# Performance work log

Measured on AMD Instinct MI355X. Metric: run time of the kernel, lower is better.

## Reference

```python
import jax, jax.numpy as jnp
import numpy as np

B, LC, LE, H, V = 128, 256, 257, 512, 128
PAD = 0  # padding_token_index


def lstm_cell(x, h, c, Wih, Whh, b):
    # torch LSTMCell gate order: i, f, g, o
    g = x @ Wih.T + h @ Whh.T + b
    i, f, gg, o = jnp.split(g, 4, axis=-1)
    c = jax.nn.sigmoid(f) * c + jax.nn.sigmoid(i) * jnp.tanh(gg)
    h = jax.nn.sigmoid(o) * jnp.tanh(c)
    return h, c


def setup_inputs() -> dict:
    key = jax.random.key(0)
    ks = jax.random.split(key, 32)
    p = lambda k, shape: jax.random.normal(k, shape, jnp.float32) * 0.05
    d = {
        'C_idx': jax.random.randint(ks[0], (B, LC), 0, V, dtype=jnp.int32),
        'E_idx': jax.random.randint(ks[1], (B, LE), 0, V, dtype=jnp.int32),
        'C_pad': jnp.zeros((B, LC), dtype=bool),
        'enc_Wih_f': p(ks[2], (4 * H, V)),
        'enc_Whh_f': p(ks[3], (4 * H, H)),
        'enc_b_f': p(ks[4], (4 * H,)),
        'enc_Wih_b': p(ks[5], (4 * H, V)),
        'enc_Whh_b': p(ks[6], (4 * H, H)),
        'enc_b_b': p(ks[7], (4 * H,)),
        'dec_Wih': p(ks[8], (4 * H, H + V)),
        'dec_Whh': p(ks[9], (4 * H, H)),
        'dec_b': p(ks[10], (4 * H,)),
        'Wh': p(ks[11], (H, 2 * H)),
        'Wc': p(ks[12], (H, 2 * H)),
        'Wattn': p(ks[13], (H, 2 * H)),
        'Wout': p(ks[14], (H, 3 * H)),
        'Wvocab': p(ks[15], (V, H)),
        'pg_ctx': p(ks[16], (2 * H,)),
        'pg_in': p(ks[17], (V + H,)),
        'pg_h': p(ks[18], (H,)),
        'pg_c': p(ks[19], (H,)),
        'pg_b': p(ks[20], (1,)),
    }
    return d


def _forward(C_idx, E_idx, C_pad, enc_Wih_f, enc_Whh_f, enc_b_f, enc_Wih_b, enc_Whh_b, enc_b_b,
             dec_Wih, dec_Whh, dec_b, Wh, Wc, Wattn, Wout, Wvocab,
             pg_ctx, pg_in, pg_h, pg_c, pg_b):
    C = jax.nn.one_hot(C_idx, V, dtype=jnp.float32)      # [B,LC,V]
    E_emb = jax.nn.one_hot(E_idx, V, dtype=jnp.float32)  # [B,LE,V]
    z = jnp.zeros((B, H), jnp.float32)

    xs = jnp.swapaxes(C, 0, 1)  # [LC,B,V]

    def enc_fwd(carry, x):
        h, c = lstm_cell(x, carry[0], carry[1], enc_Wih_f, enc_Whh_f, enc_b_f)
        return (h, c), h

    def enc_bwd(carry, x):
        h, c = lstm_cell(x, carry[0], carry[1], enc_Wih_b, enc_Whh_b, enc_b_b)
        return (h, c), h

    (hf, cf), Hf = jax.lax.scan(enc_fwd, (z, z), xs)
    (hb, cb), Hb = jax.lax.scan(enc_bwd, (z, z), xs[::-1])
    Hb = Hb[::-1]
    enc = jnp.swapaxes(jnp.concatenate([Hf, Hb], axis=-1), 0, 1)  # [B,LC,2H]

    # decoder init state from final encoder states (fwd;bwd concat)
    h0 = jnp.concatenate([hf, hb], axis=-1) @ Wh.T
    c0 = jnp.concatenate([cf, cb], axis=-1) @ Wc.T

    enc_proj = enc @ Wattn.T  # [B,LC,H]

    def step(carry, x_emb):
        h, c, prev_out = carry
        nin = jnp.concatenate([x_emb, prev_out], axis=1)  # [B,V+H]
        h, c = lstm_cell(nin, h, c, dec_Wih, dec_Whh, dec_b)
        scores = jnp.einsum('blh,bh->bl', enc_proj, h)
        scores = jnp.where(C_pad, -jnp.inf, scores)
        attn = jax.nn.softmax(scores, axis=1)             # [B,LC]
        ctx = jnp.einsum('bl,blh->bh', attn, enc)         # [B,2H]
        t_out = jnp.tanh(jnp.concatenate([h, ctx], axis=1) @ Wout.T)  # [B,H]
        gen = jax.nn.softmax(t_out @ Wvocab.T, axis=1)    # [B,V]
        p_gen = jax.nn.sigmoid(ctx @ pg_ctx + nin @ pg_in + h @ pg_h + c @ pg_c + pg_b[0])[:, None]
        copy_p = attn * (1.0 - p_gen)
        out = jax.vmap(lambda o, idx, a: o.at[idx].add(a))(gen * p_gen, C_idx, copy_p)
        return (h, c, t_out), out

    xs2 = jnp.swapaxes(E_emb[:, :LE - 1], 0, 1)  # teacher inputs, step 0 = start token
    _, preds = jax.lax.scan(step, (h0, c0, z), xs2)
    preds = jnp.swapaxes(preds, 0, 1)  # [B,LE-1,V]

    tgt = E_idx[:, 1:]
    nll = -jnp.take_along_axis(jnp.log(preds), tgt[..., None], axis=2)[..., 0]
    return jnp.where(tgt == PAD, 0.0, nll)  # [B,LE-1], reduction='none'


def reference(C_idx, E_idx, C_pad, enc_Wih_f, enc_Whh_f, enc_b_f, enc_Wih_b, enc_Whh_b, enc_b_b,
              dec_Wih, dec_Whh, dec_b, Wh, Wc, Wattn, Wout, Wvocab,
              pg_ctx, pg_in, pg_h, pg_c, pg_b):
    return _forward(C_idx, E_idx, C_pad, enc_Wih_f, enc_Whh_f, enc_b_f, enc_Wih_b, enc_Whh_b, enc_b_b,
                    dec_Wih, dec_Whh, dec_b, Wh, Wc, Wattn, Wout, Wvocab,
                    pg_ctx, pg_in, pg_h, pg_c, pg_b)
```

## Files before the change

kernel.cpp:

```cpp
#include <hip/hip_runtime.h>

static constexpr size_t OFF_ENC   = 0;
static constexpr size_t OFF_WGE   = 67108864;
static constexpr size_t OFF_WIHTE = 71303168;
static constexpr size_t OFF_HENC  = 72351744;
static constexpr size_t OFF_CENC  = 72876032;
static constexpr size_t OFF_WGATE = 67108864;
static constexpr size_t OFF_XDEC  = 71303168;
static constexpr size_t OFF_WATTT = 71827456;
static constexpr size_t OFF_WOUT  = 72876032;
static constexpr size_t OFF_WVOCT = 74448896;
static constexpr size_t OFF_HDEC  = 74579968;
static constexpr size_t OFF_CDEC  = 74842112;
static constexpr size_t OFF_TOUT  = 75104256;
static constexpr size_t OFF_UFB   = 75366400;
static constexpr size_t OFF_CTXF  = 75628544;
static constexpr size_t OFF_CTXP  = 75890688;
static constexpr size_t OFF_SC    = 76414976;
static constexpr size_t OFF_MSP   = 76480512;
static constexpr size_t OFF_MD    = 76482560;

__device__ __forceinline__ float sigm(float x) { return 1.f / (1.f + expf(-x)); }
__device__ __forceinline__ unsigned short f2bf(float f) {
  unsigned u = __float_as_uint(f);
  u += 0x7fffu + ((u >> 16) & 1u);
  return (unsigned short)(u >> 16);
}
__device__ __forceinline__ float bfl(unsigned w) { return __uint_as_float(w << 16); }
__device__ __forceinline__ float bfh(unsigned w) { return __uint_as_float(w & 0xffff0000u); }
__device__ __forceinline__ float bf2f(unsigned short v) { return __uint_as_float(((unsigned)v) << 16); }

#if defined(__has_builtin)
// ... 6 lines not shown
__device__ __forceinline__ float dot2bf(unsigned w, unsigned h, float acc) {
  return __builtin_amdgcn_fdot2_f32_bf16(__builtin_bit_cast(bf2_t, w),
                                         __builtin_bit_cast(bf2_t, h), acc, false);
}
#else
__device__ __forceinline__ float dot2bf(unsigned w, unsigned h, float acc) {
  return acc + bfl(w) * bfl(h) + bfh(w) * bfh(h);
}
#endif

__global__ __launch_bounds__(256) void k_pre1(const float* __restrict__ WhhF,
                                              const float* __restrict__ WhhB,
                                              const float* __restrict__ WihF,
                                              const float* __restrict__ WihB,
                                              char* __restrict__ wsb) {
  unsigned short* WGE = (unsigned short*)(wsb + OFF_WGE);
  unsigned short* WIH = (unsigned short*)(wsb + OFF_WIHTE);
  int id = blockIdx.x * 256 + threadIdx.x, str = gridDim.x * 256;
  for (int x = id; x < 2 * 2048 * 512; x += str) {
    int dir = x >> 20, r = (x >> 9) & 2047, k = x & 511;
    const float* W = dir ? WhhB : WhhF;
    WGE[x] = f2bf(W[(size_t)r * 512 + k]);
  }
  for (int x = id; x < 2 * 128 * 2048; x += str) {
    int dir = x >> 18, v = (x >> 11) & 127, r = x & 2047;
    const float* W = dir ? WihB : WihF;
    WIH[x] = f2bf(W[(size_t)r * 128 + v]);
  }
}

__global__ __launch_bounds__(256) void k_pre2(const float* __restrict__ dWih,
                                              const float* __restrict__ dWhh,
                                              const float* __restrict__ Wattn,
                                              const float* __restrict__ Wout,
                                              const float* __restrict__ Wvoc,
                                              char* __restrict__ wsb) {
  unsigned short* WG = (unsigned short*)(wsb + OFF_WGATE);
  unsigned short* XD = (unsigned short*)(wsb + OFF_XDEC);
  unsigned short* WA = (unsigned short*)(wsb + OFF_WATTT);
  unsigned short* WO = (unsigned short*)(wsb + OFF_WOUT);
  unsigned*       WV = (unsigned*)(wsb + OFF_WVOCT);
  int id = blockIdx.x * 256 + threadIdx.x, str = gridDim.x * 256;
  for (int x = id; x < 2048 * 1024; x += str) {
// ... 6 lines not shown
    XD[x] = f2bf(dWih[(size_t)r * 640 + v]);
  }
  for (int x = id; x < 1024 * 512; x += str) {
    int i = x >> 9, o = x & 511;
    WA[x] = f2bf(Wattn[(size_t)o * 1024 + i]);
  }
  for (int x = id; x < 512 * 1536; x += str) WO[x] = f2bf(Wout[x]);
  for (int x = id; x < 256 * 128; x += str) {
    int kk = x >> 7, v = x & 127;
    unsigned lo = f2bf(Wvoc[(size_t)v * 512 + 2 * kk]);
    unsigned hi = f2bf(Wvoc[(size_t)v * 512 + 2 * kk + 1]);
    WV[x] = lo | (hi << 16);
  }
}

__global__ __launch_bounds__(512) void k_encs(const float* __restrict__ bF,
                                              const float* __restrict__ bB,
                                              const int* __restrict__ C_idx,
                                              char* __restrict__ wsb, int t) {
  int tau = threadIdx.x, bid = blockIdx.x;
  int b = tau & 127, slot = tau >> 7;
  int dir = bid >> 7;
  int j = __builtin_amdgcn_readfirstlane(((bid & 127) << 2) + slot);
  int dd = __builtin_amdgcn_readfirstlane(dir);
  int rp = t & 1, wp = rp ^ 1;
  const unsigned* inw = (const unsigned*)(wsb + OFF_HENC) + ((size_t)(dd * 2 + rp) * 256) * 128 + b;
  const uint4* w0 = (const uint4*)((const unsigned*)(wsb + OFF_WGE) + ((size_t)dd * 2048 + j) * 256);
  const uint4* w1 = (const uint4*)((const unsigned*)(wsb + OFF_WGE) + ((size_t)dd * 2048 + 512 + j) * 256);
  const uint4* w2 = (const uint4*)((const unsigned*)(wsb + OFF_WGE) + ((size_t)dd * 2048 + 1024 + j) * 256);
  const uint4* w3 = (const uint4*)((const unsigned*)(wsb + OFF_WGE) + ((size_t)dd * 2048 + 1536 + j) * 256);
  int l = dd ? (255 - t) : t;
  int cidx = C_idx[b * 256 + l];
  const unsigned short* xg = (const unsigned short*)(wsb + OFF_WIHTE) + ((size_t)dd * 128 + cidx) * 2048;
  const float* bias = dd ? bB : bF;
  float a0 = bias[j] + bf2f(xg[j]);
  float a1 = bias[512 + j] + bf2f(xg[512 + j]);
  float a2 = bias[1024 + j] + bf2f(xg[1024 + j]);
  float a3 = bias[1536 + j] + bf2f(xg[1536 + j]);
#pragma unroll 4
  for (int q = 0; q < 64; ++q) {
    uint4 W0 = w0[q], W1 = w1[q], W2 = w2[q], W3 = w3[q];
    unsigned i0 = inw[(q * 4 + 0) * 128], i1 = inw[(q * 4 + 1) * 128];
    unsigned i2 = inw[(q * 4 + 2) * 128], i3 = inw[(q * 4 + 3) * 128];
    a0 = dot2bf(W0.x, i0, a0); a0 = dot2bf(W0.y, i1, a0); a0 = dot2bf(W0.z, i2, a0); a0 = dot2bf(W0.w, i3, a0);
    a1 = dot2bf(W1.x, i0, a1); a1 = dot2bf(W1.y, i1, a1); a1 = dot2bf(W1.z, i2, a1); a1 = dot2bf(W1.w, i3, a1);
    a2 = dot2bf(W2.x, i0, a2); a2 = dot2bf(W2.y, i1, a2); a2 = dot2bf(W2.z, i2, a2); a2 = dot2bf(W2.w, i3, a2);
    a3 = dot2bf(W3.x, i0, a3); a3 = dot2bf(W3.y, i1, a3); a3 = dot2bf(W3.z, i2, a3); a3 = dot2bf(W3.w, i3, a3);
  }
  float ig = sigm(a0), fg = sigm(a1), gg = tanhf(a2), og = sigm(a3);
  float* cp = (float*)(wsb + OFF_CENC) + ((size_t)dir * 512 + j) * 128 + b;
  float c = fg * (*cp) + ig * gg;
  *cp = c;
  float h = og * tanhf(c);
  unsigned short hb = f2bf(h);
  ((unsigned short*)(wsb + OFF_HENC))[((((size_t)(dir * 2 + wp) * 256) + (j >> 1)) * 128 + b) * 2 + (j & 1)] = hb;
  ((unsigned short*)(wsb + OFF_ENC))[((size_t)b * 256 + l) * 1024 + dir * 512 + j] = hb;
}

__global__ __launch_bounds__(512) void k_h0(const float* __restrict__ Wh,
                                            const float* __restrict__ Wc,
                                            char* __restrict__ wsb) {
  int tau = threadIdx.x;
  int b = tau & 127, slot = tau >> 7;
  int row = __builtin_amdgcn_readfirstlane(blockIdx.x * 4 + slot);
  int sel = row >> 9, j = row & 511;
  const float* W = (sel ? Wc : Wh) + (size_t)j * 1024;
  const unsigned short* HE = (const unsigned short*)(wsb + OFF_HENC);
  const float* CE = (const float*)(wsb + OFF_CENC);
  float acc = 0.f;
  for (int k = 0; k < 1024; ++k) {
    int dir = k >> 9, k5 = k & 511;
    float in;
    if (sel == 0)
      in = bf2f(HE[((((size_t)(dir * 2 + 0) * 256) + (k5 >> 1)) * 128 + b) * 2 + (k5 & 1)]);
    else
      in = CE[((size_t)dir * 512 + k5) * 128 + b];
    acc += W[k] * in;
  }
  if (sel == 0)
    ((unsigned short*)(wsb + OFF_HDEC))[(((size_t)(j >> 1)) * 128 + b) * 2 + (j & 1)] = f2bf(acc);
  else
    ((float*)(wsb + OFF_CDEC))[(size_t)j * 128 + b] = acc;
}

__global__ __launch_bounds__(512) void k_gates(const int* __restrict__ E_idx,
                                               const float* __restrict__ db,
                                               char* __restrict__ wsb, int t) {
  __shared__ float part[2][4][128];
  int tau = threadIdx.x;
  int b = tau & 127, jslot = (tau >> 7) & 1, kh = tau >> 8;
  int j = __builtin_amdgcn_readfirstlane(blockIdx.x * 2 + jslot);
  int rp = t & 1, np = rp ^ 1;
  const unsigned* inw = (const unsigned*)(wsb + (kh ? OFF_HDEC : OFF_TOUT)) + (size_t)(kh ? np * 0 + rp : rp) * 256 * 128 + b;
  const unsigned* WG = (const unsigned*)(wsb + OFF_WGATE);
  const uint4* w0 = (const uint4*)(WG + ((size_t)(0 * 512 + j)) * 512 + kh * 256);
  const uint4* w1 = (const uint4*)(WG + ((size_t)(1 * 512 + j)) * 512 + kh * 256);
  const uint4* w2 = (const uint4*)(WG + ((size_t)(2 * 512 + j)) * 512 + kh * 256);
  const uint4* w3 = (const uint4*)(WG + ((size_t)(3 * 512 + j)) * 512 + kh * 256);
  float a0 = 0.f, a1 = 0.f, a2 = 0.f, a3 = 0.f;
#pragma unroll 4
  for (int q = 0; q < 64; ++q) {
    uint4 W0 = w0[q], W1 = w1[q], W2 = w2[q], W3 = w3[q];
    unsigned i0 = inw[(q * 4 + 0) * 128], i1 = inw[(q * 4 + 1) * 128];
    unsigned i2 = inw[(q * 4 + 2) * 128], i3 = inw[(q * 4 + 3) * 128];
    a0 = dot2bf(W0.x, i0, a0); a0 = dot2bf(W0.y, i1, a0); a0 = dot2bf(W0.z, i2, a0); a0 = dot2bf(W0.w, i3, a0);
    a1 = dot2bf(W1.x, i0, a1); a1 = dot2bf(W1.y, i1, a1); a1 = dot2bf(W1.z, i2, a1); a1 = dot2bf(W1.w, i3, a1);
    a2 = dot2bf(W2.x, i0, a2); a2 = dot2bf(W2.y, i1, a2); a2 = dot2bf(W2.z, i2, a2); a2 = dot2bf(W2.w, i3, a2);
    a3 = dot2bf(W3.x, i0, a3); a3 = dot2bf(W3.y, i1, a3); a3 = dot2bf(W3.z, i2, a3); a3 = dot2bf(W3.w, i3, a3);
  }
  if (kh == 1) { part[jslot][0][b] = a0; part[jslot][1][b] = a1; part[jslot][2][b] = a2; part[jslot][3][b] = a3; }
  __syncthreads();
  if (kh == 0) {
    int xid = E_idx[b * 257 + t];
// ... 4 lines not shown
    float g3 = a3 + part[jslot][3][b] + db[1536 + j] + bf2f(xg[1536 + j]);
    float ig = sigm(g0), fg = sigm(g1), gg = tanhf(g2), og = sigm(g3);
    float* cp = (float*)(wsb + OFF_CDEC) + (size_t)j * 128 + b;
    float c = fg * (*cp) + ig * gg;
    *cp = c;
    float h = og * tanhf(c);
    ((unsigned short*)(wsb + OFF_HDEC))[(((size_t)np * 256 + (j >> 1)) * 128 + b) * 2 + (j & 1)] = f2bf(h);
  }
}

__global__ __launch_bounds__(512) void k_u(char* __restrict__ wsb, int t) {
  int tau = threadIdx.x;
  int b = tau & 127, slot = tau >> 7;
  int i = __builtin_amdgcn_readfirstlane(blockIdx.x * 4 + slot);
  int np = (t & 1) ^ 1;
  const unsigned* inw = (const unsigned*)(wsb + OFF_HDEC) + (size_t)np * 256 * 128 + b;
  const uint4* w = (const uint4*)((const unsigned*)(wsb + OFF_WATTT) + (size_t)i * 256);
  float a = 0.f;
#pragma unroll 4
  for (int q = 0; q < 64; ++q) {
    uint4 W = w[q];
    a = dot2bf(W.x, inw[(q * 4 + 0) * 128], a);
    a = dot2bf(W.y, inw[(q * 4 + 1) * 128], a);
    a = dot2bf(W.z, inw[(q * 4 + 2) * 128], a);
    a = dot2bf(W.w, inw[(q * 4 + 3) * 128], a);
  }
  ((unsigned short*)(wsb + OFF_UFB))[(((size_t)(i >> 1)) * 128 + b) * 2 + (i & 1)] = f2bf(a);
}

__global__ __launch_bounds__(256) void k_attn(const unsigned char* __restrict__ C_pad,
                                              char* __restrict__ wsb) {
  __shared__ __align__(16) unsigned short tile[32][1024];
  __shared__ __align__(16) unsigned ulds[512];
  __shared__ float sc_l[32];
  __shared__ float p_l[32];
  __shared__ float red[4];
  int bid = blockIdx.x, tau = threadIdx.x;
  int b = bid >> 1, ch = bid & 1;
  int lane = tau & 63, wv = tau >> 6;
  const unsigned* UW = (const unsigned*)(wsb + OFF_UFB) + b;
  ulds[tau] = UW[(size_t)tau * 128];
  ulds[tau + 256] = UW[(size_t)(tau + 256) * 128];
  float mold = -3.0e38f, ssum = 0.f;
  float acc0 = 0.f, acc1 = 0.f, acc2 = 0.f, acc3 = 0.f;
  unsigned short* SCp = (unsigned short*)(wsb + OFF_SC) + (size_t)b * 256;
  int L0 = ch * 128;
  for (int sub = 0; sub < 4; ++sub) {
    const uint4* src = (const uint4*)((const unsigned short*)wsb + ((size_t)b * 256 + L0 + sub * 32) * 1024);
    __syncthreads();
#pragma unroll
    for (int it = 0; it < 16; ++it) ((uint4*)tile)[it * 256 + tau] = src[it * 256 + tau];
    __syncthreads();
    const uint4* t4 = (const uint4*)tile;
    const uint4* u4 = (const uint4*)ulds;
#pragma unroll
    for (int li = 0; li < 8; ++li) {
      int l = wv * 8 + li;
      uint4 ea = t4[l * 128 + lane * 2];
      uint4 eb = t4[l * 128 + lane * 2 + 1];
      uint4 ua = u4[lane * 2];
      uint4 ub = u4[lane * 2 + 1];
      float s = 0.f;
      s = dot2bf(ea.x, ua.x, s); s = dot2bf(ea.y, ua.y, s);
      s = dot2bf(ea.z, ua.z, s); s = dot2bf(ea.w, ua.w, s);
      s = dot2bf(eb.x, ub.x, s); s = dot2bf(eb.y, ub.y, s);
      s = dot2bf(eb.z, ub.z, s); s = dot2bf(eb.w, ub.w, s);
      for (int o = 32; o; o >>= 1) s += __shfl_xor(s, o);
      if (lane == 0) {
        int gl = L0 + sub * 32 + l;
        if (C_pad[b * 256 + gl]) s = -3.0e38f;
        sc_l[l] = s;
        SCp[gl] = f2bf(s);
      }
    }
    __syncthreads();
    if (tau < 64) {
      float v = (tau < 32) ? sc_l[tau] : -3.0e38f;
      for (int o = 32; o; o >>= 1) v = fmaxf(v, __shfl_xor(v, o));
      if (tau == 0) red[0] = v;
    }
    __syncthreads();
    float mnew = fmaxf(mold, red[0]);
    float r = expf(mold - mnew);
    if (tau < 64) {
      float pv = (tau < 32) ? expf(sc_l[tau] - mnew) : 0.f;
      if (tau < 32) p_l[tau] = pv;
      for (int o = 32; o; o >>= 1) pv += __shfl_xor(pv, o);
      if (tau == 0) red[1] = pv;
    }
    __syncthreads();
    ssum = ssum * r + red[1];
    mold = mnew;
    acc0 *= r; acc1 *= r; acc2 *= r; acc3 *= r;
    const uint2* t2 = (const uint2*)tile;
#pragma unroll 8
    for (int l = 0; l < 32; ++l) {
      float pv = p_l[l];
      uint2 ev = t2[l * 256 + tau];
      acc0 += pv * bfl(ev.x); acc1 += pv * bfh(ev.x);
      acc2 += pv * bfl(ev.y); acc3 += pv * bfh(ev.y);
    }
  }
  unsigned* CP = (unsigned*)(wsb + OFF_CTXP);
  unsigned wlo = (unsigned)f2bf(acc0) | ((unsigned)f2bf(acc1) << 16);
  unsigned whi = (unsigned)f2bf(acc2) | ((unsigned)f2bf(acc3) << 16);
  CP[(((size_t)ch * 128 + b) * 1024 + tau * 4) >> 1] = wlo;
  CP[((((size_t)ch * 128 + b) * 1024 + tau * 4) >> 1) + 1] = whi;
  if (tau == 0) {
    float* MSP = (float*)(wsb + OFF_MSP);
    MSP[b * 2 + ch] = mold;
    MSP[256 + b * 2 + ch] = ssum;
  }
}

__global__ __launch_bounds__(256) void k_comb(const int* __restrict__ E_idx,
                                              const float* __restrict__ pgc,
                                              const float* __restrict__ pgi,
                                              const float* __restrict__ pgh,
                                              const float* __restrict__ pgcc,
                                              const float* __restrict__ pgb,
                                              char* __restrict__ wsb, int t) {
  __shared__ float red[4];
  int b = blockIdx.x, tau = threadIdx.x;
  int lane = tau & 63, wv = tau >> 6;
  int rp = t & 1, np = rp ^ 1;
  const float* MSP = (const float*)(wsb + OFF_MSP);
  float m0 = MSP[b * 2], m1 = MSP[b * 2 + 1];
  float s0 = MSP[256 + b * 2], s1 = MSP[256 + b * 2 + 1];
  float M = fmaxf(m0, m1);
  float e0 = expf(m0 - M), e1 = expf(m1 - M);
  float D = s0 * e0 + s1 * e1;
  float invD = 1.f / D;
  const unsigned* CP = (const unsigned*)(wsb + OFF_CTXP);
  size_t base0 = (((size_t)0 * 128 + b) * 1024 + tau * 4) >> 1;
  size_t base1 = (((size_t)1 * 128 + b) * 1024 + tau * 4) >> 1;
  unsigned c0l = CP[base0], c0h = CP[base0 + 1], c1l = CP[base1], c1h = CP[base1 + 1];
  float x0 = (bfl(c0l) * e0 + bfl(c1l) * e1) * invD;
  float x1 = (bfh(c0l) * e0 + bfh(c1l) * e1) * invD;
  float x2 = (bfl(c0h) * e0 + bfl(c1h) * e1) * invD;
  float x3 = (bfh(c0h) * e0 + bfh(c1h) * e1) * invD;
  unsigned* CF = (unsigned*)(wsb + OFF_CTXF);
  CF[((size_t)tau * 2) * 128 + b]     = (unsigned)f2bf(x0) | ((unsigned)f2bf(x1) << 16);
  CF[((size_t)tau * 2 + 1) * 128 + b] = (unsigned)f2bf(x2) | ((unsigned)f2bf(x3) << 16);
  int f0 = tau * 4;
  float pp = x0 * pgc[f0] + x1 * pgc[f0 + 1] + x2 * pgc[f0 + 2] + x3 * pgc[f0 + 3];
  if (f0 < 512) {
    const unsigned short* H = (const unsigned short*)(wsb + OFF_HDEC);
    const unsigned short* TO = (const unsigned short*)(wsb + OFF_TOUT);
    const float* C = (const float*)(wsb + OFF_CDEC);
#pragma unroll
    for (int e = 0; e < 4; ++e) {
      int f = f0 + e;
      float hv = bf2f(H[(((size_t)np * 256 + (f >> 1)) * 128 + b) * 2 + (f & 1)]);
      float pv = bf2f(TO[(((size_t)rp * 256 + (f >> 1)) * 128 + b) * 2 + (f & 1)]);
      float cv = C[(size_t)f * 128 + b];
      pp += hv * pgh[f] + cv * pgcc[f] + pv * pgi[128 + f];
    }
  }
  for (int o = 32; o; o >>= 1) pp += __shfl_xor(pp, o);
  if (lane == 0) red[wv] = pp;
  __syncthreads();
  if (tau == 0) {
    int xid = E_idx[b * 257 + t];
    float s = red[0] + red[1] + red[2] + red[3] + pgi[xid] + pgb[0];
    float* MD = (float*)(wsb + OFF_MD);
    MD[b] = M;
    MD[128 + b] = D;
    MD[256 + b] = sigm(s);
  }
}

__global__ __launch_bounds__(512) void k_wout(char* __restrict__ wsb, int t) {
  __shared__ float part[2][128];
  int tau = threadIdx.x;
  int b = tau & 127, nslot = (tau >> 7) & 1, kh = tau >> 8;
  int n = __builtin_amdgcn_readfirstlane(blockIdx.x * 2 + nslot);
  int np = (t & 1) ^ 1;
  const unsigned* HW = (const unsigned*)(wsb + OFF_HDEC) + (size_t)np * 256 * 128 + b;
  const unsigned* CW = (const unsigned*)(wsb + OFF_CTXF) + b;
  const unsigned* w = (const unsigned*)(wsb + OFF_WOUT) + (size_t)n * 768 + kh * 384;
  float a = 0.f;
  int p0 = kh * 384;
#pragma unroll 4
  for (int q = 0; q < 96; ++q) {
    uint4 W = ((const uint4*)w)[q];
#pragma unroll
    for (int e = 0; e < 4; ++e) {
      int pp = p0 + q * 4 + e;
      unsigned in = (pp < 256) ? HW[(size_t)pp * 128] : CW[(size_t)(pp - 256) * 128];
      unsigned wv = (e == 0) ? W.x : (e == 1) ? W.y : (e == 2) ? W.z : W.w;
      a = dot2bf(wv, in, a);
    }
  }
  if (kh == 1) part[nslot][b] = a;
  __syncthreads();
  if (kh == 0) {
    float tv = tanhf(a + part[nslot][b]);
    ((unsigned short*)(wsb + OFF_TOUT))[(((size_t)np * 256 + (n >> 1)) * 128 + b) * 2 + (n & 1)] = f2bf(tv);
  }
}

__global__ __launch_bounds__(256) void k_fin(const int* __restrict__ C_idx,
                                             const int* __restrict__ E_idx,
                                             char* __restrict__ wsb,
                                             float* __restrict__ out, int t) {
  __shared__ unsigned to_pld[256];
  __shared__ float lgp[2][128];
  __shared__ float lgf[128];
  __shared__ float red[8];
  int b = blockIdx.x, tau = threadIdx.x;
  int lane = tau & 63, wv = tau >> 6;
  int np = (t & 1) ^ 1;
  const unsigned* TOW = (const unsigned*)(wsb + OFF_TOUT) + (size_t)np * 256 * 128 + b;
  to_pld[tau] = TOW[(size_t)tau * 128];
  __syncthreads();
  int v = tau & 127, kh = tau >> 7;
  const unsigned* WV = (const unsigned*)(wsb + OFF_WVOCT) + v;
  float a = 0.f;
#pragma unroll 8
  for (int kkk = 0; kkk < 128; ++kkk) {
    int kk = kh * 128 + kkk;
    a = dot2bf(WV[(size_t)kk * 128], to_pld[kk], a);
  }
  lgp[kh][v] = a;
  __syncthreads();
  if (tau < 128) {
    float lg = lgp[0][tau] + lgp[1][tau];
    lgf[tau] = lg;
    float m = lg;
    for (int o = 32; o; o >>= 1) m = fmaxf(m, __shfl_xor(m, o));
    if (lane == 0) red[wv] = m;
  }
  __syncthreads();
  float mx = fmaxf(red[0], red[1]);
  if (tau < 128) {
    float e = expf(lgf[tau] - mx);
    for (int o = 32; o; o >>= 1) e += __shfl_xor(e, o);
    if (lane == 0) red[2 + wv] = e;
  }
  __syncthreads();
  const float* MD = (const float*)(wsb + OFF_MD);
  float M = MD[b], D = MD[128 + b], pg = MD[256 + b];
  int tgt = E_idx[b * 257 + t + 1];
  float cm = 0.f;
  {
    float s = bf2f(((const unsigned short*)(wsb + OFF_SC))[(size_t)b * 256 + tau]);
    if (C_idx[b * 256 + tau] == tgt) cm = expf(s - M);
  }
  for (int o = 32; o; o >>= 1) cm += __shfl_xor(cm, o);
  if (lane == 0) red[4 + wv] = cm;
  __syncthreads();
  if (tau == 0) {
    float sume = red[2] + red[3];
    float copy_raw = red[4] + red[5] + red[6] + red[7];
    float gen_tgt = expf(lgf[tgt] - mx) / sume;
    float prob = pg * gen_tgt + (1.f - pg) * copy_raw / D;
    out[b * 256 + t] = (tgt == 0) ? 0.f : -logf(prob);
  }
}

extern "C" void kernel_launch(void* const* d_in, const int* in_sizes, int n_in,
                              void* d_out, int out_size, void* d_ws, size_t ws_size,
                              hipStream_t stream) {
  (void)in_sizes; (void)n_in; (void)out_size; (void)ws_size;
  const int* C_idx = (const int*)d_in[0];
  const int* E_idx = (const int*)d_in[1];
  const unsigned char* C_pad = (const unsigned char*)d_in[2];
  const float* eWihF = (const float*)d_in[3];
  const float* eWhhF = (const float*)d_in[4];
  const float* ebF   = (const float*)d_in[5];
  const float* eWihB = (const float*)d_in[6];
  const float* eWhhB = (const float*)d_in[7];
  const float* ebB   = (const float*)d_in[8];
// ... 1 lines not shown
  const float* dWhh  = (const float*)d_in[10];
  const float* db    = (const float*)d_in[11];
  const float* Wh    = (const float*)d_in[12];
  const float* Wc    = (const float*)d_in[13];
  const float* Wattn = (const float*)d_in[14];
  const float* Wout  = (const float*)d_in[15];
  const float* Wvoc  = (const float*)d_in[16];
  const float* pgc   = (const float*)d_in[17];
  const float* pgi   = (const float*)d_in[18];
  const float* pgh   = (const float*)d_in[19];
  const float* pgcc  = (const float*)d_in[20];
  const float* pgb   = (const float*)d_in[21];
  char* wsb = (char*)d_ws;
  float* out = (float*)d_out;

  hipMemsetAsync(wsb + OFF_HENC, 0, 524288, stream);
  hipMemsetAsync(wsb + OFF_CENC, 0, 524288, stream);
  hipMemsetAsync(wsb + OFF_TOUT, 0, 262144, stream);

  k_pre1<<<256, 256, 0, stream>>>(eWhhF, eWhhB, eWihF, eWihB, wsb);
  for (int t = 0; t < 256; ++t)
    k_encs<<<256, 512, 0, stream>>>(ebF, ebB, C_idx, wsb, t);
  k_h0<<<256, 512, 0, stream>>>(Wh, Wc, wsb);
  k_pre2<<<256, 256, 0, stream>>>(dWih, dWhh, Wattn, Wout, Wvoc, wsb);
  for (int t = 0; t < 256; ++t) {
    k_gates<<<256, 512, 0, stream>>>(E_idx, db, wsb, t);
    k_u<<<256, 512, 0, stream>>>(wsb, t);
    k_attn<<<256, 256, 0, stream>>>(C_pad, wsb);
    k_comb<<<128, 256, 0, stream>>>(E_idx, pgc, pgi, pgh, pgcc, pgb, wsb, t);
    k_wout<<<256, 512, 0, stream>>>(wsb, t);
    k_fin<<<128, 256, 0, stream>>>(C_idx, E_idx, wsb, out, t);
  }
}
```

Baseline: 27.29 ms.

## Persist encoder LSTM in one kernel and fuse decoder step kernels

The 256 per-step encoder launches become one persistent kernel: each block owns one batch row and direction, keeps h in shared memory and c in registers, and reads weights relaid out gate-interleaved. The decoder step drops from six launches to four. The vocab/NLL work of the previous step runs in extra blocks of the gate kernel, and context normalisation is folded into the output projection, which shares a launch with the pointer-gen gate. This cuts launch overhead and intermediate traffic, but each encoder block now rereads the full recurrent weight matrix every step, serialising it within one block and lowering parallelism.

```diff
diff --git a/kernel.cpp b/kernel.cpp
--- a/kernel.cpp
+++ b/kernel.cpp
@@ -1,21 +1,19 @@
 #include <hip/hip_runtime.h>
 
 static constexpr size_t OFF_ENC   = 0;
-static constexpr size_t OFF_WGE   = 67108864;
-static constexpr size_t OFF_WIHTE = 71303168;
-static constexpr size_t OFF_HENC  = 72351744;
-static constexpr size_t OFF_CENC  = 72876032;
-static constexpr size_t OFF_WGATE = 67108864;
-static constexpr size_t OFF_XDEC  = 71303168;
-static constexpr size_t OFF_WATTT = 71827456;
-static constexpr size_t OFF_WOUT  = 72876032;
-static constexpr size_t OFF_WVOCT = 74448896;
-static constexpr size_t OFF_HDEC  = 74579968;
-static constexpr size_t OFF_CDEC  = 74842112;
-static constexpr size_t OFF_TOUT  = 75104256;
-static constexpr size_t OFF_UFB   = 75366400;
-static constexpr size_t OFF_CTXF  = 75628544;
-static constexpr size_t OFF_CTXP  = 75890688;
+static constexpr size_t OFF_HFIN  = 67108864;
+static constexpr size_t OFF_CFIN  = 67633152;
+static constexpr size_t OFF_TOUT  = 67108864;
+static constexpr size_t OFF_CTXP  = 67633152;
+static constexpr size_t OFF_OVL   = 68157440;
+static constexpr size_t OFF_WGATE = 68157440;
+static constexpr size_t OFF_XDEC  = 72351744;
+static constexpr size_t OFF_WATTT = 72876032;
+static constexpr size_t OFF_WOUT  = 73924608;
+static constexpr size_t OFF_WVOCT = 75497472;
+static constexpr size_t OFF_HDEC  = 75628544;
+static constexpr size_t OFF_CDEC  = 75890688;
+static constexpr size_t OFF_UFB   = 76152832;
 static constexpr size_t OFF_SC    = 76414976;
 static constexpr size_t OFF_MSP   = 76480512;
 static constexpr size_t OFF_MD    = 76482560;
@@ -52,19 +50,85 @@
                                               const float* __restrict__ WihF,
                                               const float* __restrict__ WihB,
                                               char* __restrict__ wsb) {
-  unsigned short* WGE = (unsigned short*)(wsb + OFF_WGE);
-  unsigned short* WIH = (unsigned short*)(wsb + OFF_WIHTE);
+  unsigned short* dst = (unsigned short*)(wsb + OFF_OVL);
   int id = blockIdx.x * 256 + threadIdx.x, str = gridDim.x * 256;
-  for (int x = id; x < 2 * 2048 * 512; x += str) {
-    int dir = x >> 20, r = (x >> 9) & 2047, k = x & 511;
+  for (int x = id; x < 2097152; x += str) {
+    int dir = x >> 20, r = x & 1048575;
+    int e = r & 7, j = (r >> 3) & 511, k2 = r >> 12;
+    int g = e >> 1, k = k2 * 2 + (e & 1);
     const float* W = dir ? WhhB : WhhF;
-    WGE[x] = f2bf(W[(size_t)r * 512 + k]);
-  }
-  for (int x = id; x < 2 * 128 * 2048; x += str) {
-    int dir = x >> 18, v = (x >> 11) & 127, r = x & 2047;
+    dst[x] = f2bf(W[((size_t)g * 512 + j) * 512 + k]);
+  }
+  for (int x = id; x < 524288; x += str) {
+    int dir = x >> 18, r = x & 262143;
+    int g = r & 3, j = (r >> 2) & 511, v = r >> 11;
     const float* W = dir ? WihB : WihF;
-    WIH[x] = f2bf(W[(size_t)r * 128 + v]);
-  }
+    dst[2097152 + x] = f2bf(W[((size_t)g * 512 + j) * 128 + v]);
+  }
+}
+
+__global__ __launch_bounds__(512) void k_enc(const float* __restrict__ bF,
+                                             const float* __restrict__ bB,
+                                             const int* __restrict__ C_idx,
+                                             char* __restrict__ wsb) {
+  __shared__ __align__(16) unsigned short hbf[512];
+  int bid = blockIdx.x;
+  int b = bid & 127, dir = bid >> 7;
+  int j = threadIdx.x;
+  const unsigned short* WH = (const unsigned short*)(wsb + OFF_OVL) + (size_t)dir * 1048576;
+  const unsigned short* WX = (const unsigned short*)(wsb + OFF_OVL) + 2097152 + (size_t)dir * 262144;
+  const float* bias = dir ? bB : bF;
+  float b0 = bias[j], b1 = bias[512 + j], b2 = bias[1024 + j], b3 = bias[1536 + j];
+  unsigned short* encb = (unsigned short*)wsb + (size_t)b * 262144;
+  const uint4* wp = (const uint4*)WH + j;
+  float c = 0.f, h = 0.f;
+  hbf[j] = 0;
+  __syncthreads();
+  for (int t = 0; t < 256; ++t) {
+    int l = dir ? (255 - t) : t;
+    int cidx = C_idx[b * 256 + l];
+    uint2 xg = *(const uint2*)(WX + ((size_t)cidx * 512 + j) * 4);
+    float a0 = b0 + bfl(xg.x), a1 = b1 + bfh(xg.x);
+    float a2 = b2 + bfl(xg.y), a3 = b3 + bfh(xg.y);
+    for (int k2 = 0; k2 < 256; ++k2) {
+      uint4 w = wp[(size_t)k2 * 512];
+      unsigned hp = *(const unsigned*)((const char*)hbf + k2 * 4);
+      a0 = dot2bf(w.x, hp, a0);
+      a1 = dot2bf(w.y, hp, a1);
+      a2 = dot2bf(w.z, hp, a2);
+      a3 = dot2bf(w.w, hp, a3);
+    }
+    float ig = sigm(a0), fg = sigm(a1), gg = tanhf(a2), og = sigm(a3);
+    c = fg * c + ig * gg;
+    h = og * tanhf(c);
+    __syncthreads();
+    unsigned short hb = f2bf(h);
+    hbf[j] = hb;
+    encb[(size_t)l * 1024 + dir * 512 + j] = hb;
+    __syncthreads();
+  }
+  ((float*)(wsb + OFF_HFIN))[((size_t)b * 2 + dir) * 512 + j] = h;
+  ((float*)(wsb + OFF_CFIN))[((size_t)b * 2 + dir) * 512 + j] = c;
+}
+
+__global__ __launch_bounds__(512) void k_h0(const float* __restrict__ Wh,
+                                            const float* __restrict__ Wc,
+                                            char* __restrict__ wsb) {
+  int tau = threadIdx.x;
+  int b = tau & 127, slot = tau >> 7;
+  int row = __builtin_amdgcn_readfirstlane(blockIdx.x * 4 + slot);
+  int sel = row >> 9, j = row & 511;
+  const float* W = (sel ? Wc : Wh) + (size_t)j * 1024;
+  const float* IN = (const float*)(wsb + (sel ? OFF_CFIN : OFF_HFIN)) + (size_t)b * 1024;
+  float acc = 0.f;
+  for (int k = 0; k < 1024; k += 4) {
+    float4 wf = *(const float4*)(W + k);
+    acc += wf.x * IN[k] + wf.y * IN[k + 1] + wf.z * IN[k + 2] + wf.w * IN[k + 3];
+  }
+  if (sel == 0)
+    ((unsigned short*)(wsb + OFF_HDEC))[((size_t)(j >> 1) * 128 + b) * 2 + (j & 1)] = f2bf(acc);
+  else
+    ((float*)(wsb + OFF_CDEC))[(size_t)j * 128 + b] = acc;
 }
 
 __global__ __launch_bounds__(256) void k_pre2(const float* __restrict__ dWih,
@@ -101,89 +165,81 @@
   }
 }
 
-__global__ __launch_bounds__(512) void k_encs(const float* __restrict__ bF,
-                                              const float* __restrict__ bB,
-                                              const int* __restrict__ C_idx,
-                                              char* __restrict__ wsb, int t) {
-  int tau = threadIdx.x, bid = blockIdx.x;
-  int b = tau & 127, slot = tau >> 7;
-  int dir = bid >> 7;
-  int j = __builtin_amdgcn_readfirstlane(((bid & 127) << 2) + slot);
-  int dd = __builtin_amdgcn_readfirstlane(dir);
-  int rp = t & 1, wp = rp ^ 1;
-  const unsigned* inw = (const unsigned*)(wsb + OFF_HENC) + ((size_t)(dd * 2 + rp) * 256) * 128 + b;
-  const uint4* w0 = (const uint4*)((const unsigned*)(wsb + OFF_WGE) + ((size_t)dd * 2048 + j) * 256);
-  const uint4* w1 = (const uint4*)((const unsigned*)(wsb + OFF_WGE) + ((size_t)dd * 2048 + 512 + j) * 256);
-  const uint4* w2 = (const uint4*)((const unsigned*)(wsb + OFF_WGE) + ((size_t)dd * 2048 + 1024 + j) * 256);
-  const uint4* w3 = (const uint4*)((const unsigned*)(wsb + OFF_WGE) + ((size_t)dd * 2048 + 1536 + j) * 256);
-  int l = dd ? (255 - t) : t;
-  int cidx = C_idx[b * 256 + l];
-  const unsigned short* xg = (const unsigned short*)(wsb + OFF_WIHTE) + ((size_t)dd * 128 + cidx) * 2048;
-  const float* bias = dd ? bB : bF;
-  float a0 = bias[j] + bf2f(xg[j]);
-  float a1 = bias[512 + j] + bf2f(xg[512 + j]);
-  float a2 = bias[1024 + j] + bf2f(xg[1024 + j]);
-  float a3 = bias[1536 + j] + bf2f(xg[1536 + j]);
-#pragma unroll 4
+__device__ void fin_body(const int* __restrict__ C_idx, const int* __restrict__ E_idx,
+                         char* __restrict__ wsb, float* __restrict__ out, int b, int tf) {
+  __shared__ unsigned to_pld[256];
+  __shared__ float lgp[4][128];
+  __shared__ float lgf[128];
+  __shared__ float redf[8];
+  int tau = threadIdx.x, lane = tau & 63, wv = tau >> 6;
+  int npf = (tf & 1) ^ 1;
+  const unsigned* TOW = (const unsigned*)(wsb + OFF_TOUT) + (size_t)npf * 32768 + b;
+  if (tau < 256) to_pld[tau] = TOW[(size_t)tau * 128];
+  __syncthreads();
+  int v = tau & 127, kh = tau >> 7;
+  const unsigned* WV = (const unsigned*)(wsb + OFF_WVOCT) + v;
+  float a = 0.f;
+#pragma unroll 8
   for (int q = 0; q < 64; ++q) {
-    uint4 W0 = w0[q], W1 = w1[q], W2 = w2[q], W3 = w3[q];
-    unsigned i0 = inw[(q * 4 + 0) * 128], i1 = inw[(q * 4 + 1) * 128];
-    unsigned i2 = inw[(q * 4 + 2) * 128], i3 = inw[(q * 4 + 3) * 128];
-    a0 = dot2bf(W0.x, i0, a0); a0 = dot2bf(W0.y, i1, a0); a0 = dot2bf(W0.z, i2, a0); a0 = dot2bf(W0.w, i3, a0);
-    a1 = dot2bf(W1.x, i0, a1); a1 = dot2bf(W1.y, i1, a1); a1 = dot2bf(W1.z, i2, a1); a1 = dot2bf(W1.w, i3, a1);
-    a2 = dot2bf(W2.x, i0, a2); a2 = dot2bf(W2.y, i1, a2); a2 = dot2bf(W2.z, i2, a2); a2 = dot2bf(W2.w, i3, a2);
-    a3 = dot2bf(W3.x, i0, a3); a3 = dot2bf(W3.y, i1, a3); a3 = dot2bf(W3.z, i2, a3); a3 = dot2bf(W3.w, i3, a3);
-  }
-  float ig = sigm(a0), fg = sigm(a1), gg = tanhf(a2), og = sigm(a3);
-  float* cp = (float*)(wsb + OFF_CENC) + ((size_t)dir * 512 + j) * 128 + b;
-  float c = fg * (*cp) + ig * gg;
-  *cp = c;
-  float h = og * tanhf(c);
-  unsigned short hb = f2bf(h);
-  ((unsigned short*)(wsb + OFF_HENC))[((((size_t)(dir * 2 + wp) * 256) + (j >> 1)) * 128 + b) * 2 + (j & 1)] = hb;
-  ((unsigned short*)(wsb + OFF_ENC))[((size_t)b * 256 + l) * 1024 + dir * 512 + j] = hb;
-}
-
-__global__ __launch_bounds__(512) void k_h0(const float* __restrict__ Wh,
-                                            const float* __restrict__ Wc,
-                                            char* __restrict__ wsb) {
-  int tau = threadIdx.x;
-  int b = tau & 127, slot = tau >> 7;
-  int row = __builtin_amdgcn_readfirstlane(blockIdx.x * 4 + slot);
-  int sel = row >> 9, j = row & 511;
-  const float* W = (sel ? Wc : Wh) + (size_t)j * 1024;
-  const unsigned short* HE = (const unsigned short*)(wsb + OFF_HENC);
-  const float* CE = (const float*)(wsb + OFF_CENC);
-  float acc = 0.f;
-  for (int k = 0; k < 1024; ++k) {
-    int dir = k >> 9, k5 = k & 511;
-    float in;
-    if (sel == 0)
-      in = bf2f(HE[((((size_t)(dir * 2 + 0) * 256) + (k5 >> 1)) * 128 + b) * 2 + (k5 & 1)]);
-    else
-      in = CE[((size_t)dir * 512 + k5) * 128 + b];
-    acc += W[k] * in;
-  }
-  if (sel == 0)
-    ((unsigned short*)(wsb + OFF_HDEC))[(((size_t)(j >> 1)) * 128 + b) * 2 + (j & 1)] = f2bf(acc);
-  else
-    ((float*)(wsb + OFF_CDEC))[(size_t)j * 128 + b] = acc;
-}
-
-__global__ __launch_bounds__(512) void k_gates(const int* __restrict__ E_idx,
-                                               const float* __restrict__ db,
-                                               char* __restrict__ wsb, int t) {
+    int kk = kh * 64 + q;
+    a = dot2bf(WV[(size_t)kk * 128], to_pld[kk], a);
+  }
+  lgp[kh][v] = a;
+  __syncthreads();
+  if (tau < 128) {
+    float lg = lgp[0][tau] + lgp[1][tau] + lgp[2][tau] + lgp[3][tau];
+    lgf[tau] = lg;
+    float m = lg;
+    for (int o = 32; o; o >>= 1) m = fmaxf(m, __shfl_xor(m, o));
+    if (lane == 0) redf[wv] = m;
+  }
+  __syncthreads();
+  float mx = fmaxf(redf[0], redf[1]);
+  if (tau < 128) {
+    float e = expf(lgf[tau] - mx);
+    for (int o = 32; o; o >>= 1) e += __shfl_xor(e, o);
+    if (lane == 0) redf[2 + wv] = e;
+  }
+  const float* MD = (const float*)(wsb + OFF_MD);
+  float M = MD[b], D = MD[128 + b], pg = MD[256 + b];
+  int tgt = E_idx[b * 257 + tf + 1];
+  float cm = 0.f;
+  if (tau < 256) {
+    float s = bf2f(((const unsigned short*)(wsb + OFF_SC))[(size_t)b * 256 + tau]);
+    if (C_idx[b * 256 + tau] == tgt) cm = expf(s - M);
+  }
+  for (int o = 32; o; o >>= 1) cm += __shfl_xor(cm, o);
+  if (lane == 0 && wv < 4) redf[4 + wv] = cm;
+  __syncthreads();
+  if (tau == 0) {
+    float sume = redf[2] + redf[3];
+    float copy_raw = (redf[4] + redf[5] + redf[6] + redf[7]) / D;
+    float gen_tgt = expf(lgf[tgt] - mx) / sume;
+    float prob = pg * gen_tgt + (1.f - pg) * copy_raw;
+    out[b * 256 + tf] = (tgt == 0) ? 0.f : -logf(prob);
+  }
+}
+
+__global__ __launch_bounds__(512) void k_gfin(const int* __restrict__ C_idx,
+                                              const int* __restrict__ E_idx,
+                                              const float* __restrict__ db,
+                                              char* __restrict__ wsb,
+                                              float* __restrict__ out, int t) {
+  if (blockIdx.x >= 256) {
+    if (t > 0) fin_body(C_idx, E_idx, wsb, out, blockIdx.x - 256, t - 1);
+    return;
+  }
   __shared__ float part[2][4][128];
   int tau = threadIdx.x;
   int b = tau & 127, jslot = (tau >> 7) & 1, kh = tau >> 8;
   int j = __builtin_amdgcn_readfirstlane(blockIdx.x * 2 + jslot);
   int rp = t & 1, np = rp ^ 1;
-  const unsigned* inw = (const unsigned*)(wsb + (kh ? OFF_HDEC : OFF_TOUT)) + (size_t)(kh ? np * 0 + rp : rp) * 256 * 128 + b;
+  const unsigned* inw = (const unsigned*)(wsb + (kh ? OFF_HDEC : OFF_TOUT)) + (size_t)rp * 32768 + b;
   const unsigned* WG = (const unsigned*)(wsb + OFF_WGATE);
-  const uint4* w0 = (const uint4*)(WG + ((size_t)(0 * 512 + j)) * 512 + kh * 256);
-  const uint4* w1 = (const uint4*)(WG + ((size_t)(1 * 512 + j)) * 512 + kh * 256);
-  const uint4* w2 = (const uint4*)(WG + ((size_t)(2 * 512 + j)) * 512 + kh * 256);
-  const uint4* w3 = (const uint4*)(WG + ((size_t)(3 * 512 + j)) * 512 + kh * 256);
+  const uint4* w0 = (const uint4*)(WG + (size_t)j * 512 + kh * 256);
+  const uint4* w1 = (const uint4*)(WG + ((size_t)512 + j) * 512 + kh * 256);
+  const uint4* w2 = (const uint4*)(WG + ((size_t)1024 + j) * 512 + kh * 256);
+  const uint4* w3 = (const uint4*)(WG + ((size_t)1536 + j) * 512 + kh * 256);
   float a0 = 0.f, a1 = 0.f, a2 = 0.f, a3 = 0.f;
 #pragma unroll 4
   for (int q = 0; q < 64; ++q) {
@@ -218,7 +274,7 @@
   int b = tau & 127, slot = tau >> 7;
   int i = __builtin_amdgcn_readfirstlane(blockIdx.x * 4 + slot);
   int np = (t & 1) ^ 1;
-  const unsigned* inw = (const unsigned*)(wsb + OFF_HDEC) + (size_t)np * 256 * 128 + b;
+  const unsigned* inw = (const unsigned*)(wsb + OFF_HDEC) + (size_t)np * 32768 + b;
   const uint4* w = (const uint4*)((const unsigned*)(wsb + OFF_WATTT) + (size_t)i * 256);
   float a = 0.f;
 #pragma unroll 4
@@ -232,38 +288,35 @@
   ((unsigned short*)(wsb + OFF_UFB))[(((size_t)(i >> 1)) * 128 + b) * 2 + (i & 1)] = f2bf(a);
 }
 
-__global__ __launch_bounds__(256) void k_attn(const unsigned char* __restrict__ C_pad,
+__global__ __launch_bounds__(512) void k_attn(const unsigned char* __restrict__ C_pad,
                                               char* __restrict__ wsb) {
-  __shared__ __align__(16) unsigned short tile[32][1024];
+  __shared__ __align__(16) uint4 tile4[8192];
   __shared__ __align__(16) unsigned ulds[512];
-  __shared__ float sc_l[32];
-  __shared__ float p_l[32];
+  __shared__ float sc_l[64];
+  __shared__ float p_l[64];
   __shared__ float red[4];
+  const unsigned* tl = (const unsigned*)tile4;
   int bid = blockIdx.x, tau = threadIdx.x;
   int b = bid >> 1, ch = bid & 1;
   int lane = tau & 63, wv = tau >> 6;
   const unsigned* UW = (const unsigned*)(wsb + OFF_UFB) + b;
   ulds[tau] = UW[(size_t)tau * 128];
-  ulds[tau + 256] = UW[(size_t)(tau + 256) * 128];
-  float mold = -3.0e38f, ssum = 0.f;
-  float acc0 = 0.f, acc1 = 0.f, acc2 = 0.f, acc3 = 0.f;
+  float mold = -3.0e38f, ssum = 0.f, acc0 = 0.f, acc1 = 0.f;
   unsigned short* SCp = (unsigned short*)(wsb + OFF_SC) + (size_t)b * 256;
   int L0 = ch * 128;
-  for (int sub = 0; sub < 4; ++sub) {
-    const uint4* src = (const uint4*)((const unsigned short*)wsb + ((size_t)b * 256 + L0 + sub * 32) * 1024);
+  for (int sub = 0; sub < 2; ++sub) {
+    const uint4* src = (const uint4*)((const unsigned short*)wsb + ((size_t)b * 256 + L0 + sub * 64) * 1024);
     __syncthreads();
 #pragma unroll
-    for (int it = 0; it < 16; ++it) ((uint4*)tile)[it * 256 + tau] = src[it * 256 + tau];
-    __syncthreads();
-    const uint4* t4 = (const uint4*)tile;
+    for (int it = 0; it < 16; ++it) tile4[it * 512 + tau] = src[it * 512 + tau];
+    __syncthreads();
     const uint4* u4 = (const uint4*)ulds;
+    uint4 ua = u4[lane * 2], ub = u4[lane * 2 + 1];
 #pragma unroll
     for (int li = 0; li < 8; ++li) {
       int l = wv * 8 + li;
-      uint4 ea = t4[l * 128 + lane * 2];
-      uint4 eb = t4[l * 128 + lane * 2 + 1];
-      uint4 ua = u4[lane * 2];
-      uint4 ub = u4[lane * 2 + 1];
+      uint4 ea = tile4[l * 128 + lane * 2];
+      uint4 eb = tile4[l * 128 + lane * 2 + 1];
       float s = 0.f;
       s = dot2bf(ea.x, ua.x, s); s = dot2bf(ea.y, ua.y, s);
       s = dot2bf(ea.z, ua.z, s); s = dot2bf(ea.w, ua.w, s);
@@ -271,7 +324,7 @@
       s = dot2bf(eb.z, ub.z, s); s = dot2bf(eb.w, ub.w, s);
       for (int o = 32; o; o >>= 1) s += __shfl_xor(s, o);
       if (lane == 0) {
-        int gl = L0 + sub * 32 + l;
+        int gl = L0 + sub * 64 + l;
         if (C_pad[b * 256 + gl]) s = -3.0e38f;
         sc_l[l] = s;
         SCp[gl] = f2bf(s);
@@ -279,7 +332,7 @@
     }
     __syncthreads();
     if (tau < 64) {
-      float v = (tau < 32) ? sc_l[tau] : -3.0e38f;
+      float v = sc_l[tau];
       for (int o = 32; o; o >>= 1) v = fmaxf(v, __shfl_xor(v, o));
       if (tau == 0) red[0] = v;
     }
@@ -287,29 +340,24 @@
     float mnew = fmaxf(mold, red[0]);
     float r = expf(mold - mnew);
     if (tau < 64) {
-      float pv = (tau < 32) ? expf(sc_l[tau] - mnew) : 0.f;
-      if (tau < 32) p_l[tau] = pv;
+      float pv = expf(sc_l[tau] - mnew);
+      p_l[tau] = pv;
       for (int o = 32; o; o >>= 1) pv += __shfl_xor(pv, o);
       if (tau == 0) red[1] = pv;
     }
     __syncthreads();
     ssum = ssum * r + red[1];
     mold = mnew;
-    acc0 *= r; acc1 *= r; acc2 *= r; acc3 *= r;
-    const uint2* t2 = (const uint2*)tile;
+    acc0 *= r; acc1 *= r;
 #pragma unroll 8
-    for (int l = 0; l < 32; ++l) {
+    for (int l = 0; l < 64; ++l) {
       float pv = p_l[l];
-      uint2 ev = t2[l * 256 + tau];
-      acc0 += pv * bfl(ev.x); acc1 += pv * bfh(ev.x);
-      acc2 += pv * bfl(ev.y); acc3 += pv * bfh(ev.y);
-    }
-  }
-  unsigned* CP = (unsigned*)(wsb + OFF_CTXP);
-  unsigned wlo = (unsigned)f2bf(acc0) | ((unsigned)f2bf(acc1) << 16);
-  unsigned whi = (unsigned)f2bf(acc2) | ((unsigned)f2bf(acc3) << 16);
-  CP[(((size_t)ch * 128 + b) * 1024 + tau * 4) >> 1] = wlo;
-  CP[((((size_t)ch * 128 + b) * 1024 + tau * 4) >> 1) + 1] = whi;
+      unsigned ev = tl[l * 512 + tau];
+      acc0 += pv * bfl(ev); acc1 += pv * bfh(ev);
+    }
+  }
+  ((unsigned*)(wsb + OFF_CTXP))[((size_t)ch * 128 + b) * 512 + tau] =
+      (unsigned)f2bf(acc0) | ((unsigned)f2bf(acc1) << 16);
   if (tau == 0) {
     float* MSP = (float*)(wsb + OFF_MSP);
     MSP[b * 2 + ch] = mold;
@@ -317,71 +365,68 @@
   }
 }
 
-__global__ __launch_bounds__(256) void k_comb(const int* __restrict__ E_idx,
-                                              const float* __restrict__ pgc,
-                                              const float* __restrict__ pgi,
-                                              const float* __restrict__ pgh,
-                                              const float* __restrict__ pgcc,
-                                              const float* __restrict__ pgb,
-                                              char* __restrict__ wsb, int t) {
-  __shared__ float red[4];
-  int b = blockIdx.x, tau = threadIdx.x;
+__global__ __launch_bounds__(512) void k_wpg(const int* __restrict__ E_idx,
+                                             const float* __restrict__ pgc,
+                                             const float* __restrict__ pgi,
+                                             const float* __restrict__ pgh,
+                                             const float* __restrict__ pgcc,
+                                             const float* __restrict__ pgb,
+                                             char* __restrict__ wsb, int t) {
+  __shared__ float part[2][128];
+  __shared__ float red[8];
+  int tau = threadIdx.x;
   int lane = tau & 63, wv = tau >> 6;
   int rp = t & 1, np = rp ^ 1;
+  if (blockIdx.x >= 256) {
+    int b = blockIdx.x - 256;
+    const float* MSP = (const float*)(wsb + OFF_MSP);
+    float m0 = MSP[b * 2], m1 = MSP[b * 2 + 1];
+    float s0 = MSP[256 + b * 2], s1 = MSP[256 + b * 2 + 1];
+    float M = fmaxf(m0, m1);
+    float e0 = expf(m0 - M), e1 = expf(m1 - M);
+    float D = s0 * e0 + s1 * e1;
+    float invD = 1.f / D;
+    const unsigned* CP0 = (const unsigned*)(wsb + OFF_CTXP) + (size_t)b * 512;
+    const unsigned* CP1 = CP0 + 65536;
+    unsigned c0 = CP0[tau], c1 = CP1[tau];
+    float x0 = (bfl(c0) * e0 + bfl(c1) * e1) * invD;
+    float x1 = (bfh(c0) * e0 + bfh(c1) * e1) * invD;
+    float pp = x0 * pgc[2 * tau] + x1 * pgc[2 * tau + 1];
+    {
+      int f = tau;
+      const unsigned short* H = (const unsigned short*)(wsb + OFF_HDEC) + (size_t)np * 65536;
+      const unsigned short* TOp = (const unsigned short*)(wsb + OFF_TOUT) + (size_t)rp * 65536;
+      const float* C = (const float*)(wsb + OFF_CDEC);
+      float hv = bf2f(H[((size_t)(f >> 1) * 128 + b) * 2 + (f & 1)]);
+      float tv = bf2f(TOp[((size_t)(f >> 1) * 128 + b) * 2 + (f & 1)]);
+      float cv = C[(size_t)f * 128 + b];
+      pp += hv * pgh[f] + cv * pgcc[f] + tv * pgi[128 + f];
+    }
+    for (int o = 32; o; o >>= 1) pp += __shfl_xor(pp, o);
+    if (lane == 0) red[wv] = pp;
+    __syncthreads();
+    if (tau == 0) {
+      float s = red[0] + red[1] + red[2] + red[3] + red[4] + red[5] + red[6] + red[7];
+      s += pgi[E_idx[b * 257 + t]] + pgb[0];
+      float* MD = (float*)(wsb + OFF_MD);
+      MD[b] = M;
+      MD[128 + b] = D;
+      MD[256 + b] = sigm(s);
+    }
+    return;
+  }
+  int b = tau & 127, nslot = (tau >> 7) & 1, kh = tau >> 8;
+  int n = __builtin_amdgcn_readfirstlane(blockIdx.x * 2 + nslot);
   const float* MSP = (const float*)(wsb + OFF_MSP);
   float m0 = MSP[b * 2], m1 = MSP[b * 2 + 1];
   float s0 = MSP[256 + b * 2], s1 = MSP[256 + b * 2 + 1];
   float M = fmaxf(m0, m1);
   float e0 = expf(m0 - M), e1 = expf(m1 - M);
-  float D = s0 * e0 + s1 * e1;
-  float invD = 1.f / D;
-  const unsigned* CP = (const unsigned*)(wsb + OFF_CTXP);
-  size_t base0 = (((size_t)0 * 128 + b) * 1024 + tau * 4) >> 1;
-  size_t base1 = (((size_t)1 * 128 + b) * 1024 + tau * 4) >> 1;
-  unsigned c0l = CP[base0], c0h = CP[base0 + 1], c1l = CP[base1], c1h = CP[base1 + 1];
-  float x0 = (bfl(c0l) * e0 + bfl(c1l) * e1) * invD;
-  float x1 = (bfh(c0l) * e0 + bfh(c1l) * e1) * invD;
-  float x2 = (bfl(c0h) * e0 + bfl(c1h) * e1) * invD;
-  float x3 = (bfh(c0h) * e0 + bfh(c1h) * e1) * invD;
-  unsigned* CF = (unsigned*)(wsb + OFF_CTXF);
-  CF[((size_t)tau * 2) * 128 + b]     = (unsigned)f2bf(x0) | ((unsigned)f2bf(x1) << 16);
-  CF[((size_t)tau * 2 + 1) * 128 + b] = (unsigned)f2bf(x2) | ((unsigned)f2bf(x3) << 16);
-  int f0 = tau * 4;
-  float pp = x0 * pgc[f0] + x1 * pgc[f0 + 1] + x2 * pgc[f0 + 2] + x3 * pgc[f0 + 3];
-  if (f0 < 512) {
-    const unsigned short* H = (const unsigned short*)(wsb + OFF_HDEC);
-    const unsigned short* TO = (const unsigned short*)(wsb + OFF_TOUT);
-    const float* C = (const float*)(wsb + OFF_CDEC);
-#pragma unroll
-    for (int e = 0; e < 4; ++e) {
-      int f = f0 + e;
-      float hv = bf2f(H[(((size_t)np * 256 + (f >> 1)) * 128 + b) * 2 + (f & 1)]);
-      float pv = bf2f(TO[(((size_t)rp * 256 + (f >> 1)) * 128 + b) * 2 + (f & 1)]);
-      float cv = C[(size_t)f * 128 + b];
-      pp += hv * pgh[f] + cv * pgcc[f] + pv * pgi[128 + f];
-    }
-  }
-  for (int o = 32; o; o >>= 1) pp += __shfl_xor(pp, o);
-  if (lane == 0) red[wv] = pp;
-  __syncthreads();
-  if (tau == 0) {
-    int xid = E_idx[b * 257 + t];
-    float s = red[0] + red[1] + red[2] + red[3] + pgi[xid] + pgb[0];
-    float* MD = (float*)(wsb + OFF_MD);
-    MD[b] = M;
-    MD[128 + b] = D;
-    MD[256 + b] = sigm(s);
-  }
-}
-
-__global__ __launch_bounds__(512) void k_wout(char* __restrict__ wsb, int t) {
-  __shared__ float part[2][128];
-  int tau = threadIdx.x;
-  int b = tau & 127, nslot = (tau >> 7) & 1, kh = tau >> 8;
-  int n = __builtin_amdgcn_readfirstlane(blockIdx.x * 2 + nslot);
-  int np = (t & 1) ^ 1;
-  const unsigned* HW = (const unsigned*)(wsb + OFF_HDEC) + (size_t)np * 256 * 128 + b;
-  const unsigned* CW = (const unsigned*)(wsb + OFF_CTXF) + b;
+  float invD = 1.f / (s0 * e0 + s1 * e1);
+  e0 *= invD; e1 *= invD;
+  const unsigned* HW = (const unsigned*)(wsb + OFF_HDEC) + (size_t)np * 32768 + b;
+  const unsigned* CP0 = (const unsigned*)(wsb + OFF_CTXP) + (size_t)b * 512;
+  const unsigned* CP1 = CP0 + 65536;
   const unsigned* w = (const unsigned*)(wsb + OFF_WOUT) + (size_t)n * 768 + kh * 384;
   float a = 0.f;
   int p0 = kh * 384;
@@ -391,9 +436,16 @@
 #pragma unroll
     for (int e = 0; e < 4; ++e) {
       int pp = p0 + q * 4 + e;
-      unsigned in = (pp < 256) ? HW[(size_t)pp * 128] : CW[(size_t)(pp - 256) * 128];
-      unsigned wv = (e == 0) ? W.x : (e == 1) ? W.y : (e == 2) ? W.z : W.w;
-      a = dot2bf(wv, in, a);
+      unsigned wvv = (e == 0) ? W.x : (e == 1) ? W.y : (e == 2) ? W.z : W.w;
+      if (pp < 256) {
+        a = dot2bf(wvv, HW[(size_t)pp * 128], a);
+      } else {
+        int ci = pp - 256;
+        unsigned c0 = CP0[ci], c1 = CP1[ci];
+        float x0 = bfl(c0) * e0 + bfl(c1) * e1;
+        float x1 = bfh(c0) * e0 + bfh(c1) * e1;
+        a += bfl(wvv) * x0 + bfh(wvv) * x1;
+      }
     }
   }
   if (kh == 1) part[nslot][b] = a;
@@ -404,63 +456,11 @@
   }
 }
 
-__global__ __launch_bounds__(256) void k_fin(const int* __restrict__ C_idx,
-                                             const int* __restrict__ E_idx,
-                                             char* __restrict__ wsb,
-                                             float* __restrict__ out, int t) {
-  __shared__ unsigned to_pld[256];
-  __shared__ float lgp[2][128];
-  __shared__ float lgf[128];
-  __shared__ float red[8];
-  int b = blockIdx.x, tau = threadIdx.x;
-  int lane = tau & 63, wv = tau >> 6;
-  int np = (t & 1) ^ 1;
-  const unsigned* TOW = (const unsigned*)(wsb + OFF_TOUT) + (size_t)np * 256 * 128 + b;
-  to_pld[tau] = TOW[(size_t)tau * 128];
-  __syncthreads();
-  int v = tau & 127, kh = tau >> 7;
-  const unsigned* WV = (const unsigned*)(wsb + OFF_WVOCT) + v;
-  float a = 0.f;
-#pragma unroll 8
-  for (int kkk = 0; kkk < 128; ++kkk) {
-    int kk = kh * 128 + kkk;
-    a = dot2bf(WV[(size_t)kk * 128], to_pld[kk], a);
-  }
-  lgp[kh][v] = a;
-  __syncthreads();
-  if (tau < 128) {
-    float lg = lgp[0][tau] + lgp[1][tau];
-    lgf[tau] = lg;
-    float m = lg;
-    for (int o = 32; o; o >>= 1) m = fmaxf(m, __shfl_xor(m, o));
-    if (lane == 0) red[wv] = m;
-  }
-  __syncthreads();
-  float mx = fmaxf(red[0], red[1]);
-  if (tau < 128) {
-    float e = expf(lgf[tau] - mx);
-    for (int o = 32; o; o >>= 1) e += __shfl_xor(e, o);
-    if (lane == 0) red[2 + wv] = e;
-  }
-  __syncthreads();
-  const float* MD = (const float*)(wsb + OFF_MD);
-  float M = MD[b], D = MD[128 + b], pg = MD[256 + b];
-  int tgt = E_idx[b * 257 + t + 1];
-  float cm = 0.f;
-  {
-    float s = bf2f(((const unsigned short*)(wsb + OFF_SC))[(size_t)b * 256 + tau]);
-    if (C_idx[b * 256 + tau] == tgt) cm = expf(s - M);
-  }
-  for (int o = 32; o; o >>= 1) cm += __shfl_xor(cm, o);
-  if (lane == 0) red[4 + wv] = cm;
-  __syncthreads();
-  if (tau == 0) {
-    float sume = red[2] + red[3];
-    float copy_raw = red[4] + red[5] + red[6] + red[7];
-    float gen_tgt = expf(lgf[tgt] - mx) / sume;
-    float prob = pg * gen_tgt + (1.f - pg) * copy_raw / D;
-    out[b * 256 + t] = (tgt == 0) ? 0.f : -logf(prob);
-  }
+__global__ __launch_bounds__(512) void k_fin_last(const int* __restrict__ C_idx,
+                                                  const int* __restrict__ E_idx,
+                                                  char* __restrict__ wsb,
+                                                  float* __restrict__ out) {
+  fin_body(C_idx, E_idx, wsb, out, blockIdx.x, 255);
 }
 
 extern "C" void kernel_launch(void* const* d_in, const int* in_sizes, int n_in,
@@ -492,21 +492,16 @@
   char* wsb = (char*)d_ws;
   float* out = (float*)d_out;
 
-  hipMemsetAsync(wsb + OFF_HENC, 0, 524288, stream);
-  hipMemsetAsync(wsb + OFF_CENC, 0, 524288, stream);
-  hipMemsetAsync(wsb + OFF_TOUT, 0, 262144, stream);
-
   k_pre1<<<256, 256, 0, stream>>>(eWhhF, eWhhB, eWihF, eWihB, wsb);
-  for (int t = 0; t < 256; ++t)
-    k_encs<<<256, 512, 0, stream>>>(ebF, ebB, C_idx, wsb, t);
+  k_enc<<<256, 512, 0, stream>>>(ebF, ebB, C_idx, wsb);
   k_h0<<<256, 512, 0, stream>>>(Wh, Wc, wsb);
+  hipMemsetAsync(wsb + OFF_TOUT, 0, 524288, stream);
   k_pre2<<<256, 256, 0, stream>>>(dWih, dWhh, Wattn, Wout, Wvoc, wsb);
   for (int t = 0; t < 256; ++t) {
-    k_gates<<<256, 512, 0, stream>>>(E_idx, db, wsb, t);
+    k_gfin<<<384, 512, 0, stream>>>(C_idx, E_idx, db, wsb, out, t);
     k_u<<<256, 512, 0, stream>>>(wsb, t);
-    k_attn<<<256, 256, 0, stream>>>(C_pad, wsb);
-    k_comb<<<128, 256, 0, stream>>>(E_idx, pgc, pgi, pgh, pgcc, pgb, wsb, t);
-    k_wout<<<256, 512, 0, stream>>>(wsb, t);
-    k_fin<<<128, 256, 0, stream>>>(C_idx, E_idx, wsb, out, t);
-  }
-}
+    k_attn<<<256, 512, 0, stream>>>(C_pad, wsb);
+    k_wpg<<<384, 512, 0, stream>>>(E_idx, pgc, pgi, pgh, pgcc, pgb, wsb, t);
+  }
+  k_fin_last<<<128, 512, 0, stream>>>(C_idx, E_idx, wsb, out);
+}
```

New measurement: 69.80 ms. 156% more time.
